# Optimization experiments

Hardware: AMD Instinct MI355X
Metric: run time of the kernel (lower is better)

The kernel has to match this reference:

```python
import jax, jax.numpy as jnp
import numpy as np

POS_SIZE = 63
LATENT_SIZE = 256
NUM_CLUSTERS = 64
N = 524288


def setup_inputs() -> dict:
    key = jax.random.key(0)
    k1, k2, k3, k4 = jax.random.split(key, 4)
    X = jax.random.normal(k1, (N, POS_SIZE + LATENT_SIZE), dtype=jnp.float32)
    cluster_ids = jax.random.randint(k2, (N,), 0, NUM_CLUSTERS, dtype=jnp.int32)
    # nn.Linear weights have shape [out_features, in_features]
    W_pos = jax.random.normal(k3, (3 * NUM_CLUSTERS, POS_SIZE), dtype=jnp.float32) * 0.1
    W_feat = jax.random.normal(k4, (3 * NUM_CLUSTERS, LATENT_SIZE), dtype=jnp.float32) * 0.1
    return {"X": X, "cluster_ids": cluster_ids, "W_pos": W_pos, "W_feat": W_feat}


def reference(X, cluster_ids, W_pos, W_feat):
    # Dense projections: [N, 3*num_clusters]
    rgb_clusters = (
        jnp.einsum("np,cp->nc", X[:, :POS_SIZE], W_pos)
        + jnp.einsum("nl,cl->nc", X[:, POS_SIZE:], W_feat)
    )
    # Per-row gather of the 3 columns belonging to this row's cluster.
    cols = 3 * cluster_ids[:, None] + jnp.arange(3, dtype=cluster_ids.dtype)[None, :]  # [N, 3]
    rgb = jnp.take_along_axis(rgb_clusters, cols, axis=1)  # [N, 3]
    return rgb
```

## Files before the change

### kernel.cpp

```cpp
#include <hip/hip_runtime.h>


constexpr int POS = 63;
constexpr int LAT = 256;
constexpr int DIM = POS + LAT;
constexpr int NCLUST = 64;
constexpr int WPAD = 320;
constexpr int HB = 256;

constexpr size_t WCAT_ELEMS = (size_t)192 * WPAD;
constexpr size_t HIST_OFF = WCAT_ELEMS * 4;
constexpr size_t OFF_OFF  = HIST_OFF + 64 * 4;
constexpr size_t PERM_OFF = OFF_OFF + 64 * 4;
static size_t ws_needed(int n) { return PERM_OFF + (size_t)n * 4; }

__global__ __launch_bounds__(256) void init_wcat(
    const float* __restrict__ Wp,
    const float* __restrict__ Wf,
    float* __restrict__ wcat, int* __restrict__ hist)
{
    const int idx = blockIdx.x * 256 + threadIdx.x;
    if (idx < NCLUST) hist[idx] = 0;
    if (idx >= (int)WCAT_ELEMS) return;
    const int ch = idx / WPAD, k = idx % WPAD;
    float w = 0.f;
    if (k < POS)            w = Wp[ch * POS + k];
    else if (k < DIM)       w = Wf[ch * LAT + (k - POS)];
    wcat[idx] = w;
}

__global__ __launch_bounds__(256) void hist_kernel(
    const int* __restrict__ cid, int n, int* __restrict__ hist)
{
    __shared__ int h[NCLUST];
    const int t = threadIdx.x;
    if (t < NCLUST) h[t] = 0;
    __syncthreads();
    const int chunk = (n + HB - 1) / HB;
    const int lo = blockIdx.x * chunk;
    const int hi = min(lo + chunk, n);
    for (int i = lo + t; i < hi; i += 256)
        atomicAdd(&h[cid[i]], 1);
    __syncthreads();
    if (t < NCLUST) atomicAdd(&hist[t], h[t]);
}

__global__ void scan_kernel(const int* __restrict__ hist, int* __restrict__ off)
{
    if (threadIdx.x == 0 && blockIdx.x == 0) {
        int acc = 0;
        for (int c = 0; c < NCLUST; ++c) { off[c] = acc; acc += hist[c]; }
    }
}

__global__ __launch_bounds__(256) void scatter_kernel(
    const int* __restrict__ cid, int n, int* __restrict__ off,
    int* __restrict__ perm)
{
    __shared__ int h[NCLUST];
    const int t = threadIdx.x;
    if (t < NCLUST) h[t] = 0;
    __syncthreads();
    const int chunk = (n + HB - 1) / HB;
    const int lo = blockIdx.x * chunk;
    const int hi = min(lo + chunk, n);
    for (int i = lo + t; i < hi; i += 256)
        atomicAdd(&h[cid[i]], 1);
    __syncthreads();
    if (t < NCLUST) h[t] = atomicAdd(&off[t], h[t]);
    __syncthreads();
    for (int i = lo + t; i < hi; i += 256) {
        const int c = cid[i];
        const int p = atomicAdd(&h[c], 1);
        perm[p] = i;
    }
}

template <int CTRL>
__device__ __forceinline__ float dpp_add_step(float x) {
    int s = __builtin_amdgcn_update_dpp(0, __float_as_int(x), CTRL,
                                        0xF, 0xF, true);
    return x + __int_as_float(s);
}
__device__ __forceinline__ float wave_reduce_sum(float x) {
    x = dpp_add_step<0x111>(x);
    x = dpp_add_step<0x112>(x);
    x = dpp_add_step<0x114>(x);
    x = dpp_add_step<0x118>(x);
    x = dpp_add_step<0x142>(x);
    x = dpp_add_step<0x143>(x);
    return x;
}

__global__ __launch_bounds__(256) void lad_binned(
    const float* __restrict__ X,
    const int*   __restrict__ cid,
    const int*   __restrict__ perm,
    const float* __restrict__ wcat,
    float*       __restrict__ out,
    int n)
{
    const int l   = threadIdx.x & 63;
    const int wid = (int)((blockIdx.x * blockDim.x + threadIdx.x) >> 6);
    const int base = wid * 64;
    if (base >= n) return;

    int vperm = 0, vcid = 0;
    if (base + l < n) { vperm = perm[base + l]; vcid = cid[vperm]; }

    int cur = -1;
    float w0[5], w1[5], w2[5];

    const int cnt = min(64, n - base);
    for (int j = 0; j < cnt; ++j) {
        const int r = __builtin_amdgcn_readlane(vperm, j);
        const int c = __builtin_amdgcn_readlane(vcid, j);
        if (c != cur) {
            cur = c;
            const float* wb = wcat + (size_t)(3 * c) * WPAD + l;
#pragma unroll
            for (int i = 0; i < 5; ++i) {
                w0[i] = wb[i * 64];
                w1[i] = wb[WPAD + i * 64];
                w2[i] = wb[2 * WPAD + i * 64];
            }
        }
        const float* xr = X + (size_t)r * DIM + l;
        float a0 = 0.f, a1 = 0.f, a2 = 0.f;
#pragma unroll
        for (int i = 0; i < 4; ++i) {
            const float x = xr[i * 64];
            a0 = fmaf(x, w0[i], a0);
            a1 = fmaf(x, w1[i], a1);
            a2 = fmaf(x, w2[i], a2);
        }
        {
            const float x = (l < 63) ? xr[256] : 0.f;
            a0 = fmaf(x, w0[4], a0);
            a1 = fmaf(x, w1[4], a1);
            a2 = fmaf(x, w2[4], a2);
        }
        a0 = wave_reduce_sum(a0);
        a1 = wave_reduce_sum(a1);
        a2 = wave_reduce_sum(a2);
        if (l == 63) {
            float* o = out + (size_t)r * 3;
            o[0] = a0; o[1] = a1; o[2] = a2;
        }
    }
}

__global__ __launch_bounds__(256) void lad_fallback(
    const float* __restrict__ X,
    const int*   __restrict__ cid,
    const float* __restrict__ Wp,
    const float* __restrict__ Wf,
    float*       __restrict__ out,
    int n)
{
    const int lane = threadIdx.x & 63;
    const int wave = (int)((blockIdx.x * blockDim.x + threadIdx.x) >> 6);
    if (wave >= n) return;
    const size_t row = (size_t)wave;
    const float* xrow = X + row * (size_t)DIM;
    const float* xf   = xrow + POS;
    const int c3 = cid[row] * 3;
    const float* wp0 = Wp + (size_t)c3 * POS;
    const float* wf0 = Wf + (size_t)c3 * LAT;
    float a0 = 0.f, a1 = 0.f, a2 = 0.f;
#pragma unroll
    for (int i = 0; i < 4; ++i) {
        const int k = lane + 64 * i;
        const float x = xf[k];
        a0 = fmaf(x, wf0[k], a0);
        a1 = fmaf(x, wf0[k + LAT], a1);
        a2 = fmaf(x, wf0[k + 2 * LAT], a2);
    }
    if (lane < POS) {
        const float x = xrow[lane];
        a0 = fmaf(x, wp0[lane], a0);
        a1 = fmaf(x, wp0[lane + POS], a1);
        a2 = fmaf(x, wp0[lane + 2 * POS], a2);
    }
    a0 = wave_reduce_sum(a0);
    a1 = wave_reduce_sum(a1);
    a2 = wave_reduce_sum(a2);
    if (lane == 63) {
        float* o = out + row * 3;
        o[0] = a0; o[1] = a1; o[2] = a2;
    }
}

extern "C" void kernel_launch(void* const* d_in, const int* in_sizes, int n_in,
                              void* d_out, int out_size, void* d_ws, size_t ws_size,
                              hipStream_t stream) {
    const float* X   = (const float*)d_in[0];
    const int*   cid = (const int*)d_in[1];
    const float* Wp  = (const float*)d_in[2];
    const float* Wf  = (const float*)d_in[3];
    float* out = (float*)d_out;
    const int n = in_sizes[1];

    if (ws_size >= ws_needed(n)) {
        char* ws = (char*)d_ws;
        float* wcat = (float*)ws;
        int*   hist = (int*)(ws + HIST_OFF);
        int*   off  = (int*)(ws + OFF_OFF);
        int*   perm = (int*)(ws + PERM_OFF);

        const int init_blocks = ((int)WCAT_ELEMS + 255) / 256;
        init_wcat<<<init_blocks, 256, 0, stream>>>(Wp, Wf, wcat, hist);
        hist_kernel<<<HB, 256, 0, stream>>>(cid, n, hist);
        scan_kernel<<<1, 64, 0, stream>>>(hist, off);
        scatter_kernel<<<HB, 256, 0, stream>>>(cid, n, off, perm);

        const int waves = (n + 63) / 64;
        const int blocks = (waves + 3) / 4;
        lad_binned<<<blocks, 256, 0, stream>>>(X, cid, perm, wcat, out, n);
    } else {
        const int blocks = (n + 3) / 4;
        lad_fallback<<<blocks, 256, 0, stream>>>(X, cid, Wp, Wf, out, n);
    }
}
```

Before: 173.1 us.

## Pack cluster id into perm entries and software-pipeline row loads

The scatter pass now stores the cluster id in the top 8 bits of each perm entry, so the main kernel no longer does a dependent gather of cid. The main loop also prefetches the next row of X into registers while the current row is reduced, and uses nontemporal loads for X. This targets memory latency in the per-row serial loop. In exchange it uses more registers and assumes row indices fit in 24 bits, which holds for N=524288.

```diff
diff --git a/kernel.cpp b/kernel.cpp
--- a/kernel.cpp
+++ b/kernel.cpp
@@ -3,7 +3,7 @@
 
 constexpr int POS = 63;
 constexpr int LAT = 256;
-constexpr int DIM = POS + LAT;
+constexpr int DIM = 319;
 constexpr int NCLUST = 64;
 constexpr int WPAD = 320;
 constexpr int HB = 256;
@@ -55,7 +55,7 @@
 
 __global__ __launch_bounds__(256) void scatter_kernel(
     const int* __restrict__ cid, int n, int* __restrict__ off,
-    int* __restrict__ perm)
+    unsigned* __restrict__ perm)
 {
     __shared__ int h[NCLUST];
     const int t = threadIdx.x;
@@ -72,7 +72,7 @@
     for (int i = lo + t; i < hi; i += 256) {
         const int c = cid[i];
         const int p = atomicAdd(&h[c], 1);
-        perm[p] = i;
+        perm[p] = ((unsigned)c << 24) | (unsigned)i;
     }
 }
 
@@ -92,10 +92,9 @@
     return x;
 }
 
-__global__ __launch_bounds__(256) void lad_binned(
+__global__ __launch_bounds__(256) void lad_binned2(
     const float* __restrict__ X,
-    const int*   __restrict__ cid,
-    const int*   __restrict__ perm,
+    const unsigned* __restrict__ perm,
     const float* __restrict__ wcat,
     float*       __restrict__ out,
     int n)
@@ -105,19 +104,43 @@
     const int base = wid * 64;
     if (base >= n) return;
 
-    int vperm = 0, vcid = 0;
-    if (base + l < n) { vperm = perm[base + l]; vcid = cid[vperm]; }
+    unsigned vp = 0;
+    if (base + l < n) vp = perm[base + l];
+    const int cnt = min(64, n - base);
+
+    unsigned pk = __builtin_amdgcn_readlane(vp, 0);
+    int r_cur = (int)(pk & 0xFFFFFFu);
+    int c_cur = (int)(pk >> 24);
+    {
+    }
+    const float* xr0 = X + (size_t)r_cur * DIM + l;
+    float xa0 = __builtin_nontemporal_load(xr0);
+    float xa1 = __builtin_nontemporal_load(xr0 + 64);
+    float xa2 = __builtin_nontemporal_load(xr0 + 128);
+    float xa3 = __builtin_nontemporal_load(xr0 + 192);
+    float xa4 = (l < 63) ? __builtin_nontemporal_load(xr0 + 256) : 0.f;
 
     int cur = -1;
     float w0[5], w1[5], w2[5];
 
-    const int cnt = min(64, n - base);
     for (int j = 0; j < cnt; ++j) {
-        const int r = __builtin_amdgcn_readlane(vperm, j);
-        const int c = __builtin_amdgcn_readlane(vcid, j);
-        if (c != cur) {
-            cur = c;
-            const float* wb = wcat + (size_t)(3 * c) * WPAD + l;
+        int r_nxt = 0, c_nxt = 0;
+        float xb0 = 0.f, xb1 = 0.f, xb2 = 0.f, xb3 = 0.f, xb4 = 0.f;
+        if (j + 1 < cnt) {
+            const unsigned pkn = __builtin_amdgcn_readlane(vp, j + 1);
+            r_nxt = (int)(pkn & 0xFFFFFFu);
+            c_nxt = (int)(pkn >> 24);
+            const float* xn = X + (size_t)r_nxt * DIM + l;
+            xb0 = __builtin_nontemporal_load(xn);
+            xb1 = __builtin_nontemporal_load(xn + 64);
+            xb2 = __builtin_nontemporal_load(xn + 128);
+            xb3 = __builtin_nontemporal_load(xn + 192);
+            if (l < 63) xb4 = __builtin_nontemporal_load(xn + 256);
+        }
+
+        if (c_cur != cur) {
+            cur = c_cur;
+            const float* wb = wcat + (size_t)(3 * cur) * WPAD + l;
 #pragma unroll
             for (int i = 0; i < 5; ++i) {
                 w0[i] = wb[i * 64];
@@ -125,28 +148,25 @@
                 w2[i] = wb[2 * WPAD + i * 64];
             }
         }
-        const float* xr = X + (size_t)r * DIM + l;
-        float a0 = 0.f, a1 = 0.f, a2 = 0.f;
-#pragma unroll
-        for (int i = 0; i < 4; ++i) {
-            const float x = xr[i * 64];
-            a0 = fmaf(x, w0[i], a0);
-            a1 = fmaf(x, w1[i], a1);
-            a2 = fmaf(x, w2[i], a2);
-        }
-        {
-            const float x = (l < 63) ? xr[256] : 0.f;
-            a0 = fmaf(x, w0[4], a0);
-            a1 = fmaf(x, w1[4], a1);
-            a2 = fmaf(x, w2[4], a2);
-        }
+
+        float a0 = xa0 * w0[0];
+        float a1 = xa0 * w1[0];
+        float a2 = xa0 * w2[0];
+        a0 = fmaf(xa1, w0[1], a0); a1 = fmaf(xa1, w1[1], a1); a2 = fmaf(xa1, w2[1], a2);
+        a0 = fmaf(xa2, w0[2], a0); a1 = fmaf(xa2, w1[2], a1); a2 = fmaf(xa2, w2[2], a2);
+        a0 = fmaf(xa3, w0[3], a0); a1 = fmaf(xa3, w1[3], a1); a2 = fmaf(xa3, w2[3], a2);
+        a0 = fmaf(xa4, w0[4], a0); a1 = fmaf(xa4, w1[4], a1); a2 = fmaf(xa4, w2[4], a2);
+
         a0 = wave_reduce_sum(a0);
         a1 = wave_reduce_sum(a1);
         a2 = wave_reduce_sum(a2);
         if (l == 63) {
-            float* o = out + (size_t)r * 3;
+            float* o = out + (size_t)r_cur * 3;
             o[0] = a0; o[1] = a1; o[2] = a2;
         }
+
+        r_cur = r_nxt; c_cur = c_nxt;
+        xa0 = xb0; xa1 = xb1; xa2 = xb2; xa3 = xb3; xa4 = xb4;
     }
 }
 
@@ -203,10 +223,10 @@
 
     if (ws_size >= ws_needed(n)) {
         char* ws = (char*)d_ws;
-        float* wcat = (float*)ws;
-        int*   hist = (int*)(ws + HIST_OFF);
-        int*   off  = (int*)(ws + OFF_OFF);
-        int*   perm = (int*)(ws + PERM_OFF);
+        float*    wcat = (float*)ws;
+        int*      hist = (int*)(ws + HIST_OFF);
+        int*      off  = (int*)(ws + OFF_OFF);
+        unsigned* perm = (unsigned*)(ws + PERM_OFF);
 
         const int init_blocks = ((int)WCAT_ELEMS + 255) / 256;
         init_wcat<<<init_blocks, 256, 0, stream>>>(Wp, Wf, wcat, hist);
@@ -216,7 +236,7 @@
 
         const int waves = (n + 63) / 64;
         const int blocks = (waves + 3) / 4;
-        lad_binned<<<blocks, 256, 0, stream>>>(X, cid, perm, wcat, out, n);
+        lad_binned2<<<blocks, 256, 0, stream>>>(X, perm, wcat, out, n);
     } else {
         const int blocks = (n + 3) / 4;
         lad_fallback<<<blocks, 256, 0, stream>>>(X, cid, Wp, Wf, out, n);
```

After: 178.8 us. 3.3% more time.
